# Kernel tuning notes

Measured on AMD Instinct MI355X. Metric: run time of the kernel, lower is better.

The kernel has to match this reference:

```python
import jax, jax.numpy as jnp
import numpy as np

N = 100000      # nodes
E = 3200000     # edges
G = 512         # graphs
F = 12          # num_features
NHID = 64
HGCN = NHID - 3   # 61, GCNConv output dim
EMB_OUT = 64 - F + 2  # 54


def _p(key, shape, scale):
    return jax.random.normal(key, shape, jnp.float32) * scale


def setup_inputs() -> dict:
    key = jax.random.key(0)
    ks = jax.random.split(key, 24)
    inp = {}
    inp["x"] = jax.random.normal(ks[0], (N, F), jnp.float32)
    inp["edge_index"] = jax.random.randint(ks[1], (2, E), 0, N)
    inp["batch"] = jnp.sort(jax.random.randint(ks[2], (N,), 0, G))
    inp["known_mask"] = jax.random.randint(ks[3], (E // 3,), 0, E)
    inp["unk_mask"] = jax.random.randint(ks[4], (E // 3,), 0, E)
    inp["obs_mask"] = jax.random.randint(ks[5], (E // 3,), 0, E)
    inp["fn_averages"] = jax.random.normal(ks[6], (G, 2), jnp.float32)
    inp["infection_rates"] = jax.random.normal(ks[7], (G, 1), jnp.float32)
    # parameters
    inp["msg_weights"] = jax.random.normal(ks[8], (3,), jnp.float32)
    inp["W_emb"] = _p(ks[9], (2, EMB_OUT), 0.5)
    inp["b_emb"] = jnp.zeros((EMB_OUT,), jnp.float32)
    inp["W_gcn"] = _p(ks[10], (64, HGCN), 0.125)
    inp["b_gcn"] = jnp.zeros((HGCN,), jnp.float32)
    inp["W_fn1"] = _p(ks[11], (3, 16), 0.5)
    inp["b_fn1"] = jnp.zeros((16,), jnp.float32)
    inp["W_fn2"] = _p(ks[12], (16, 3), 0.25)
    inp["b_fn2"] = jnp.zeros((3,), jnp.float32)
    inp["W_bb1"] = _p(ks[13], (NHID, NHID), 0.125)
    inp["b_bb1"] = jnp.zeros((NHID,), jnp.float32)
    inp["W_out"] = _p(ks[14], (NHID, 1), 0.125)
    inp["b_out"] = jnp.zeros((1,), jnp.float32)
    return inp


def reference(x, edge_index, batch, known_mask, unk_mask, obs_mask,
              fn_averages, infection_rates, msg_weights,
              W_emb, b_emb, W_gcn, b_gcn, W_fn1, b_fn1, W_fn2, b_fn2,
              W_bb1, b_bb1, W_out, b_out):
    gelu = lambda t: jax.nn.gelu(t, approximate=False)
    n = x.shape[0]
    e = edge_index.shape[1]
    g = fn_averages.shape[0]

    sp = jax.nn.softmax(msg_weights)
    ew = jnp.ones((e,), x.dtype)
    ew = ew.at[known_mask].set(sp[0]).at[unk_mask].set(sp[1]).at[obs_mask].set(sp[2])

    # node embedding: Linear on first 2 feats, concat rest -> (N, 64)
    h = jnp.concatenate([x[:, :2] @ W_emb + b_emb, x[:, 2:]], axis=1)

    # GCNConv(64 -> 61) with edge weights and self-loops
    h = h @ W_gcn                                  # (N, HGCN) transform first
    row, col = edge_index[0], edge_index[1]
    loop = jnp.arange(n)
    row_f = jnp.concatenate([row, loop])
    col_f = jnp.concatenate([col, loop])
    ew_f = jnp.concatenate([ew, jnp.ones((n,), ew.dtype)])
    deg = jax.ops.segment_sum(ew_f, col_f, num_segments=n)   # weighted in-degree
    dis = jnp.where(deg > 0, jax.lax.rsqrt(jnp.maximum(deg, 1e-12)), 0.0)
    norm = dis[row_f] * ew_f * dis[col_f]                    # (E+N,)
    out = jax.ops.segment_sum(norm[:, None] * h[row_f], col_f, num_segments=n)
    out = gelu(out + b_gcn)                                  # dropout = identity (eval)

    # global_add_pool over graphs
    pooled = jax.ops.segment_sum(out, batch, num_segments=g)  # (G, HGCN)

    # fn embeddings MLP on (fn_averages, infection_rate)
    extra = jnp.concatenate([fn_averages.reshape(-1, 2),
                             infection_rates.reshape(-1, 1)], axis=1)  # (G, 3)
    fn_e = gelu(extra @ W_fn1 + b_fn1) @ W_fn2 + b_fn2        # (G, 3)

    z = jnp.concatenate([pooled, fn_e], axis=1)               # (G, NHID)
    z = gelu(z @ W_bb1 + b_bb1)
    logits = z @ W_out + b_out                                # (G, 1)
    return logits
```

## Files before the change

### kernel.cpp

```cpp
#include <hip/hip_runtime.h>
#include <hip/hip_fp16.h>
#include <math.h>

#define F_IN 12
#define NHID 64
#define HGCN 61
#define EMB_OUT 54
#define SCAN_CH 1024
#define PART_R 8192
#define DEG_SCALE 32768.0f
#define NRM_SCALE 32768.0f

typedef unsigned int uint;
typedef unsigned short ushort;
typedef unsigned char uchar;

__device__ __forceinline__ float gelu_exact(float v) {
    return 0.5f * v * (1.0f + erff(v * 0.70710678118654752440f));
}

__device__ __forceinline__ void atomic_add_f32(float* p, float v) {
    unsafeAtomicAdd(p, v);
}

__global__ void prep_kernel(const float* __restrict__ msg_w,
                            const float* __restrict__ W_emb,
                            const float* __restrict__ b_emb,
                            const float* __restrict__ W_gcn,
                            float* __restrict__ sp, uint* __restrict__ spq,
                            float* __restrict__ W_eff, float* __restrict__ b_eff) {
    __shared__ float ssp[4];
    int t = threadIdx.x;
    if (t == 0) {
        float m = fmaxf(msg_w[0], fmaxf(msg_w[1], msg_w[2]));
        float e0 = expf(msg_w[0] - m), e1 = expf(msg_w[1] - m), e2 = expf(msg_w[2] - m);
        float s = e0 + e1 + e2;
        ssp[0] = 1.0f; ssp[1] = e0 / s; ssp[2] = e1 / s; ssp[3] = e2 / s;
        sp[0] = ssp[0]; sp[1] = ssp[1]; sp[2] = ssp[2]; sp[3] = ssp[3];
    }
    __syncthreads();
    if (t < 4) spq[t] = __float2uint_rn(ssp[t] * DEG_SCALE);
    if (t < HGCN) {
        float be = 0.f, w0 = 0.f, w1 = 0.f;
        for (int k = 0; k < EMB_OUT; ++k) {
            float g = W_gcn[k * HGCN + t];
            be += b_emb[k] * g;
            w0 += W_emb[k] * g;
            w1 += W_emb[EMB_OUT + k] * g;
        }
        b_eff[t] = be;
        W_eff[0 * 64 + t] = w0;
        W_eff[1 * 64 + t] = w1;
        for (int f = 2; f < F_IN; ++f)
            W_eff[f * 64 + t] = W_gcn[(EMB_OUT + f - 2) * HGCN + t];
    }
}

__global__ void set_mask_u8(uchar* __restrict__ wclass, const int* __restrict__ mask,
                            uchar v, int n) {
    int i = blockIdx.x * blockDim.x + threadIdx.x;
    if (i < n) wclass[mask[i]] = v;
}

__global__ __launch_bounds__(256) void k1_hist(const int* __restrict__ ei,
                                               uint* __restrict__ H,
                                               uchar* __restrict__ wclass,
                                               int E, int NB, int NBLK) {
    __shared__ uint hist[512];
    int blk = blockIdx.x, t = threadIdx.x;
    hist[t] = 0; hist[t + 256] = 0;
    __syncthreads();
    int lo = blk * PART_R, hi = min(lo + PART_R, E);
    for (int i = lo + t; i < hi; i += 256) {
        wclass[i] = 0;
        atomicAdd(&hist[((uint)ei[E + i]) >> 8], 1u);
    }
    __syncthreads();
    for (int b = t; b < NB; b += 256) H[(size_t)b * NBLK + blk] = hist[b];
}

__global__ void scan_partial_kernel(const int* __restrict__ cnt, int* __restrict__ startv,
                                    int* __restrict__ bsum, int n) {
    __shared__ int s[256];
    int t = threadIdx.x;
    int base = blockIdx.x * SCAN_CH + t * 4;
    int v0 = (base + 0 < n) ? cnt[base + 0] : 0;
    int v1 = (base + 1 < n) ? cnt[base + 1] : 0;
    int v2 = (base + 2 < n) ? cnt[base + 2] : 0;
    int v3 = (base + 3 < n) ? cnt[base + 3] : 0;
    int loc = v0 + v1 + v2 + v3;
    s[t] = loc;
    __syncthreads();
    for (int off = 1; off < 256; off <<= 1) {
        int u = (t >= off) ? s[t - off] : 0;
        __syncthreads();
        s[t] += u;
        __syncthreads();
    }
    int ex = s[t] - loc;
    if (t == 255) bsum[blockIdx.x] = s[255];
    if (base + 0 < n) startv[base + 0] = ex;
    if (base + 1 < n) startv[base + 1] = ex + v0;
    if (base + 2 < n) startv[base + 2] = ex + v0 + v1;
    if (base + 3 < n) startv[base + 3] = ex + v0 + v1 + v2;
}

__global__ void scan_add_kernel(int* __restrict__ startv, const int* __restrict__ bsum, int n) {
    __shared__ int soff;
    int b = blockIdx.x;
    if (threadIdx.x == 0) {
        int q = (b * 256) / SCAN_CH;
        int acc = 0;
        for (int j = 0; j < q; ++j) acc += bsum[j];
        soff = acc;
    }
    __syncthreads();
    int i = b * 256 + threadIdx.x;
    if (i < n) startv[i] += soff;
}

__global__ __launch_bounds__(256) void k3_partition(
        const int* __restrict__ ei, const uchar* __restrict__ wclass,
        const uint* __restrict__ Hs, uint* __restrict__ recSorted,
        int E, int NB, int NBLK) {
    __shared__ uint recs[PART_R];
    __shared__ ushort sbkt[PART_R];
    __shared__ uint hist[512];
    __shared__ uint scanA[512];
    __shared__ uint scanB[512];
    __shared__ int  gbase[512];
    __shared__ uint cursor[512];
    int blk = blockIdx.x, t = threadIdx.x;
    int lo = blk * PART_R, hi = min(lo + PART_R, E);
    int cntTot = hi - lo;
    hist[t] = 0; hist[t + 256] = 0;
    __syncthreads();
    for (int i = lo + t; i < hi; i += 256)
        atomicAdd(&hist[((uint)ei[E + i]) >> 8], 1u);
    __syncthreads();
    uint* src = scanA; uint* dst = scanB;
    src[t] = hist[t]; src[t + 256] = hist[t + 256];
    __syncthreads();
    for (int off = 1; off < 512; off <<= 1) {
        dst[t]       = src[t]       + ((t >= off)       ? src[t - off]       : 0u);
        dst[t + 256] = src[t + 256] + ((t + 256 >= off) ? src[t + 256 - off] : 0u);
        __syncthreads();
        uint* tmp = src; src = dst; dst = tmp;
    }
    uint l0 = (t == 0) ? 0u : src[t - 1];
    uint l1 = src[t + 255];
    cursor[t] = l0; cursor[t + 256] = l1;
    if (t < NB)       gbase[t]       = (int)Hs[(size_t)t * NBLK + blk]         - (int)l0;
    if (t + 256 < NB) gbase[t + 256] = (int)Hs[(size_t)(t + 256) * NBLK + blk] - (int)l1;
    __syncthreads();
    for (int i = lo + t; i < hi; i += 256) {
        uint row = (uint)ei[i];
        uint col = (uint)ei[E + i];
        uint b = col >> 8;
        uint rec = (row << 10) | ((col & 255u) << 2) | (uint)wclass[i];
        uint slot = atomicAdd(&cursor[b], 1u);
        recs[slot] = rec;
        sbkt[slot] = (ushort)b;
    }
    __syncthreads();
    for (int s = t; s < cntTot; s += 256)
        recSorted[gbase[sbkt[s]] + s] = recs[s];
}

__global__ __launch_bounds__(256) void k2_stats(
        const uint* __restrict__ recSorted, const uint* __restrict__ Hs,
        const uint* __restrict__ spq,
        uint* __restrict__ cnt, uint* __restrict__ startv, float* __restrict__ dis,
        int E, int NB, int NBLK, int n_nodes) {
    __shared__ uint hcnt[256], hdeg[256], sA[256], sB[256];
    __shared__ uint sq[4];
    int b = blockIdx.x, t = threadIdx.x;
    hcnt[t] = 0; hdeg[t] = 0;
    if (t < 4) sq[t] = spq[t];
    __syncthreads();
    uint lo = Hs[(size_t)b * NBLK];
    uint hi = (b + 1 < NB) ? Hs[(size_t)(b + 1) * NBLK] : (uint)E;
    for (uint i = lo + t; i < hi; i += 256) {
        uint r = recSorted[i];
        atomicAdd(&hcnt[(r >> 2) & 255u], 1u);
        atomicAdd(&hdeg[(r >> 2) & 255u], sq[r & 3u]);
    }
    __syncthreads();
    uint* src = sA; uint* dst = sB;
    src[t] = hcnt[t];
    __syncthreads();
    for (int off = 1; off < 256; off <<= 1) {
        dst[t] = src[t] + ((t >= off) ? src[t - off] : 0u);
        __syncthreads();
        uint* tmp = src; src = dst; dst = tmp;
    }
    uint excl = (t == 0) ? 0u : src[t - 1];
    int node = (b << 8) + t;
    if (node < n_nodes) {
        cnt[node] = hcnt[t];
        startv[node] = lo + excl;
        float deg = (float)hdeg[t] * (1.0f / DEG_SCALE) + 1.0f;
        dis[node] = rsqrtf(deg);
    }
}

__global__ __launch_bounds__(256) void k4_payload(
        const uint* __restrict__ recSorted, const uint* __restrict__ Hs,
        const float* __restrict__ sp, const float* __restrict__ dis,
        const uint* __restrict__ startv,
        uint* __restrict__ payload, int E, int NB, int NBLK, int n_nodes) {
    __shared__ float disl[256];
    __shared__ uint cur[256];
    __shared__ float spl[4];
    int b = blockIdx.x, t = threadIdx.x;
    int node = (b << 8) + t;
    disl[t] = (node < n_nodes) ? dis[node] : 0.0f;
    cur[t]  = (node < n_nodes) ? startv[node] : 0u;
    if (t < 4) spl[t] = sp[t];
    __syncthreads();
    uint lo = Hs[(size_t)b * NBLK];
    uint hi = (b + 1 < NB) ? Hs[(size_t)(b + 1) * NBLK] : (uint)E;
    for (uint i = lo + t; i < hi; i += 256) {
        uint r = recSorted[i];
        uint row = r >> 10;
        uint c = (r >> 2) & 255u;
        float nrm = dis[row] * spl[r & 3u] * disl[c];
        uint pos = atomicAdd(&cur[c], 1u);
        payload[pos] = (row << 15) | __float2uint_rn(nrm * NRM_SCALE);
    }
}

__global__ void h2_kernel(const float* __restrict__ x, const float* __restrict__ W_eff,
                          const float* __restrict__ b_eff,
                          __half* __restrict__ h2, float* __restrict__ pooled, int g64,
                          int n_nodes) {
    int gid = blockIdx.x * 256 + threadIdx.x;
    if (gid < g64) pooled[gid] = 0.0f;
    int node = blockIdx.x * 4 + (threadIdx.x >> 6);
    int d = threadIdx.x & 63;
    if (node >= n_nodes) return;
    float v = 0.f;
    if (d < HGCN) {
        v = b_eff[d];
#pragma unroll
        for (int f = 0; f < F_IN; ++f)
            v += x[node * F_IN + f] * W_eff[f * 64 + d];
    }
    h2[node * 64 + d] = __float2half(v);
}

__global__ void gather_pool_kernel(const uint* __restrict__ payload,
                                   const uint* __restrict__ startv, const uint* __restrict__ cnt,
                                   const float* __restrict__ dis,
                                   const __half2* __restrict__ h2v,
                                   const float* __restrict__ b_gcn, const int* __restrict__ batch,
                                   float* __restrict__ pooled, int n_nodes) {
    int node = blockIdx.x * 4 + (threadIdx.x >> 6);
    int lane = threadIdx.x & 63;
    int g = lane >> 5;
    int sub = lane & 31;
    if (node >= n_nodes) return;
    int s = (int)startv[node];
    int m = (int)cnt[node];
    const float inv = 1.0f / NRM_SCALE;
    float accx = 0.f, accy = 0.f;
    if (g == 0) {
        float di = dis[node];
        float2 hv = __half22float2(h2v[node * 32 + sub]);
        accx = di * di * hv.x;
        accy = di * di * hv.y;
    }
    for (int j0 = 0; j0 < m; j0 += 64) {
        uint p = 0;
        if (j0 + lane < m) p = payload[s + j0 + lane];
        int lim = min(64, m - j0);
        int npairs = (lim + 1) >> 1;
        int k = 0;
        for (; k + 8 <= npairs; k += 8) {
            uint p0 = __shfl(p, 2 * (k + 0) + g);
            uint p1 = __shfl(p, 2 * (k + 1) + g);
            uint p2 = __shfl(p, 2 * (k + 2) + g);
            uint p3 = __shfl(p, 2 * (k + 3) + g);
            uint p4 = __shfl(p, 2 * (k + 4) + g);
            uint p5 = __shfl(p, 2 * (k + 5) + g);
            uint p6 = __shfl(p, 2 * (k + 6) + g);
            uint p7 = __shfl(p, 2 * (k + 7) + g);
            float2 h0 = __half22float2(h2v[(p0 >> 15) * 32 + sub]);
            float2 h1 = __half22float2(h2v[(p1 >> 15) * 32 + sub]);
            float2 h2f = __half22float2(h2v[(p2 >> 15) * 32 + sub]);
            float2 h3 = __half22float2(h2v[(p3 >> 15) * 32 + sub]);
            float2 h4 = __half22float2(h2v[(p4 >> 15) * 32 + sub]);
            float2 h5 = __half22float2(h2v[(p5 >> 15) * 32 + sub]);
            float2 h6 = __half22float2(h2v[(p6 >> 15) * 32 + sub]);
            float2 h7 = __half22float2(h2v[(p7 >> 15) * 32 + sub]);
            float w0 = (float)(p0 & 32767u) * inv;
            float w1 = (float)(p1 & 32767u) * inv;
            float w2 = (float)(p2 & 32767u) * inv;
            float w3 = (float)(p3 & 32767u) * inv;
            float w4 = (float)(p4 & 32767u) * inv;
            float w5 = (float)(p5 & 32767u) * inv;
            float w6 = (float)(p6 & 32767u) * inv;
            float w7 = (float)(p7 & 32767u) * inv;
            accx += w0 * h0.x; accy += w0 * h0.y;
            accx += w1 * h1.x; accy += w1 * h1.y;
            accx += w2 * h2f.x; accy += w2 * h2f.y;
            accx += w3 * h3.x; accy += w3 * h3.y;
            accx += w4 * h4.x; accy += w4 * h4.y;
            accx += w5 * h5.x; accy += w5 * h5.y;
            accx += w6 * h6.x; accy += w6 * h6.y;
            accx += w7 * h7.x; accy += w7 * h7.y;
        }
        for (; k < npairs; ++k) {
            uint pk = __shfl(p, 2 * k + g);
            float2 hk = __half22float2(h2v[(pk >> 15) * 32 + sub]);
            float wk = (float)(pk & 32767u) * inv;
            accx += wk * hk.x; accy += wk * hk.y;
        }
    }
    accx += __shfl_xor(accx, 32);
    accy += __shfl_xor(accy, 32);
    int d = 2 * sub + g;
    float val = g ? accy : accx;
    if (d < HGCN) {
        float v = gelu_exact(val + b_gcn[d]);
        atomic_add_f32(&pooled[batch[node] * 64 + d], v);
    }
}

__global__ void final_kernel(const float* __restrict__ pooled,
                             const float* __restrict__ fn_avg,
                             const float* __restrict__ inf_rate,
                             const float* __restrict__ W_fn1, const float* __restrict__ b_fn1,
                             const float* __restrict__ W_fn2, const float* __restrict__ b_fn2,
                             const float* __restrict__ W_bb1, const float* __restrict__ b_bb1,
                             const float* __restrict__ W_out, const float* __restrict__ b_out,
                             float* __restrict__ logits) {
    __shared__ float z[64];
    __shared__ float t1[16];
    int g = blockIdx.x;
    int t = threadIdx.x;
    if (t < HGCN) z[t] = pooled[g * 64 + t];
    float e0 = fn_avg[g * 2], e1 = fn_avg[g * 2 + 1], e2 = inf_rate[g];
    if (t < 16) {
        float a = e0 * W_fn1[t] + e1 * W_fn1[16 + t] + e2 * W_fn1[32 + t] + b_fn1[t];
        t1[t] = gelu_exact(a);
    }
    __syncthreads();
    if (t < 3) {
        float a = b_fn2[t];
#pragma unroll
        for (int k = 0; k < 16; ++k) a += t1[k] * W_fn2[k * 3 + t];
        z[HGCN + t] = a;
    }
    __syncthreads();
    float acc = b_bb1[t];
#pragma unroll 8
    for (int k = 0; k < 64; ++k) acc += z[k] * W_bb1[k * 64 + t];
    float p = gelu_exact(acc) * W_out[t];
#pragma unroll
    for (int off = 32; off > 0; off >>= 1) p += __shfl_down(p, off);
    if (t == 0) logits[g] = p + b_out[0];
}

extern "C" void kernel_launch(void* const* d_in, const int* in_sizes, int n_in,
                              void* d_out, int out_size, void* d_ws, size_t ws_size,
                              hipStream_t stream) {
    const float* x        = (const float*)d_in[0];
    const int*   ei       = (const int*)d_in[1];
    const int*   batch    = (const int*)d_in[2];
    const int*   known    = (const int*)d_in[3];
    const int*   unk      = (const int*)d_in[4];
    const int*   obs      = (const int*)d_in[5];
    const float* fn_avg   = (const float*)d_in[6];
    const float* inf_rate = (const float*)d_in[7];
    const float* msg_w    = (const float*)d_in[8];
    const float* W_emb    = (const float*)d_in[9];
    const float* b_emb    = (const float*)d_in[10];
    const float* W_gcn    = (const float*)d_in[11];
    const float* b_gcn    = (const float*)d_in[12];
    const float* W_fn1    = (const float*)d_in[13];
    const float* b_fn1    = (const float*)d_in[14];
    const float* W_fn2    = (const float*)d_in[15];
    const float* b_fn2    = (const float*)d_in[16];
    const float* W_bb1    = (const float*)d_in[17];
    const float* b_bb1    = (const float*)d_in[18];
    const float* W_out    = (const float*)d_in[19];
    const float* b_out    = (const float*)d_in[20];
    float* logits = (float*)d_out;

    const int n_nodes = in_sizes[0] / F_IN;
    const int E       = in_sizes[1] / 2;
    const int nk = in_sizes[3], nu = in_sizes[4], no = in_sizes[5];
    const int G = in_sizes[6] / 2;

    const int NB   = (n_nodes + 255) >> 8;
    const int NBLK = (E + PART_R - 1) / PART_R;
    const int L    = NB * NBLK;
    const int nbL  = (L + SCAN_CH - 1) / SCAN_CH;

    char* ws = (char*)d_ws;
    size_t off = 0;
    auto alloc = [&](size_t bytes) -> void* {
        void* p = ws + off;
        off += (bytes + 255) & ~size_t(255);
        return p;
    };
    uchar*  wclass    = (uchar*)alloc(sizeof(uchar) * (size_t)E);
    uint*   recSorted = (uint*)alloc(sizeof(uint) * (size_t)E);
    uint*   H         = (uint*)alloc(sizeof(uint) * (size_t)L);
    uint*   Hs        = (uint*)alloc(sizeof(uint) * (size_t)L);
    int*    bsum      = (int*)alloc(sizeof(int) * (size_t)(nbL + 1));
    __half* h2        = (__half*)alloc(sizeof(__half) * (size_t)n_nodes * 64);
    uint*   payload   = (uint*)alloc(sizeof(uint) * (size_t)E);
    uint*   cntv      = (uint*)alloc(sizeof(uint) * (size_t)n_nodes);
    uint*   startv    = (uint*)alloc(sizeof(uint) * (size_t)n_nodes);
    float*  dis       = (float*)alloc(sizeof(float) * (size_t)n_nodes);
    float*  pooled    = (float*)alloc(sizeof(float) * (size_t)G * 64);
    float*  W_eff     = (float*)alloc(sizeof(float) * F_IN * 64);
    float*  b_eff     = (float*)alloc(sizeof(float) * 64);
    float*  sp        = (float*)alloc(sizeof(float) * 4);
    uint*   spq       = (uint*)alloc(sizeof(uint) * 4);

    prep_kernel<<<1, 64, 0, stream>>>(msg_w, W_emb, b_emb, W_gcn, sp, spq, W_eff, b_eff);
    k1_hist<<<NBLK, 256, 0, stream>>>(ei, H, wclass, E, NB, NBLK);
    set_mask_u8<<<(nk + 255) / 256, 256, 0, stream>>>(wclass, known, 1, nk);
    set_mask_u8<<<(nu + 255) / 256, 256, 0, stream>>>(wclass, unk, 2, nu);
    set_mask_u8<<<(no + 255) / 256, 256, 0, stream>>>(wclass, obs, 3, no);
    scan_partial_kernel<<<nbL, 256, 0, stream>>>((const int*)H, (int*)Hs, bsum, L);
    scan_add_kernel<<<(L + 255) / 256, 256, 0, stream>>>((int*)Hs, bsum, L);
    k3_partition<<<NBLK, 256, 0, stream>>>(ei, wclass, Hs, recSorted, E, NB, NBLK);
    k2_stats<<<NB, 256, 0, stream>>>(recSorted, Hs, spq, cntv, startv, dis, E, NB, NBLK, n_nodes);
    h2_kernel<<<(n_nodes + 3) / 4, 256, 0, stream>>>(x, W_eff, b_eff, h2, pooled, G * 64, n_nodes);
    k4_payload<<<NB, 256, 0, stream>>>(recSorted, Hs, sp, dis, startv, payload, E, NB, NBLK, n_nodes);
    gather_pool_kernel<<<(n_nodes + 3) / 4, 256, 0, stream>>>(payload, startv, cntv, dis,
                                                              (const __half2*)h2, b_gcn, batch,
                                                              pooled, n_nodes);
    final_kernel<<<G, 64, 0, stream>>>(pooled, fn_avg, inf_rate, W_fn1, b_fn1,
                                       W_fn2, b_fn2, W_bb1, b_bb1, W_out, b_out, logits);
}
```

Measured before the change: 241.9 us.

## Fold degree normalization into node features and merge prep into histogram kernel

Factors the symmetric normalization dis[row]*w*dis[col] so that dis[row] is applied once per source node in h2 and dis[col] once per destination after aggregation. The edge payload then stores only the quantized class weight, which removes the random dis[row] gather per edge in k4_payload. The one-block prep kernel is also merged into block 0 of the histogram kernel, saving a launch. The class weight is quantized at a 16384 scale, and pre-scaling h2 in fp16 changes where rounding happens.

```diff
diff --git a/kernel.cpp b/kernel.cpp
--- a/kernel.cpp
+++ b/kernel.cpp
@@ -9,7 +9,7 @@
 #define SCAN_CH 1024
 #define PART_R 8192
 #define DEG_SCALE 32768.0f
-#define NRM_SCALE 32768.0f
+#define W_SCALE 16384.0f
 
 typedef unsigned int uint;
 typedef unsigned short ushort;
@@ -23,60 +23,57 @@
     unsafeAtomicAdd(p, v);
 }
 
-__global__ void prep_kernel(const float* __restrict__ msg_w,
-                            const float* __restrict__ W_emb,
-                            const float* __restrict__ b_emb,
-                            const float* __restrict__ W_gcn,
-                            float* __restrict__ sp, uint* __restrict__ spq,
-                            float* __restrict__ W_eff, float* __restrict__ b_eff) {
+__global__ __launch_bounds__(256) void k1_hist_prep(
+        const int* __restrict__ ei, uint* __restrict__ H, uchar* __restrict__ wclass,
+        const float* __restrict__ msg_w, const float* __restrict__ W_emb,
+        const float* __restrict__ b_emb, const float* __restrict__ W_gcn,
+        uint* __restrict__ spq, uint* __restrict__ sq15,
+        float* __restrict__ W_eff, float* __restrict__ b_eff,
+        int E, int NB, int NBLK) {
+    __shared__ uint hist[512];
     __shared__ float ssp[4];
-    int t = threadIdx.x;
-    if (t == 0) {
+    int blk = blockIdx.x, t = threadIdx.x;
+    hist[t] = 0; hist[t + 256] = 0;
+    if (blk == 0 && t == 0) {
         float m = fmaxf(msg_w[0], fmaxf(msg_w[1], msg_w[2]));
         float e0 = expf(msg_w[0] - m), e1 = expf(msg_w[1] - m), e2 = expf(msg_w[2] - m);
         float s = e0 + e1 + e2;
         ssp[0] = 1.0f; ssp[1] = e0 / s; ssp[2] = e1 / s; ssp[3] = e2 / s;
-        sp[0] = ssp[0]; sp[1] = ssp[1]; sp[2] = ssp[2]; sp[3] = ssp[3];
-    }
-    __syncthreads();
-    if (t < 4) spq[t] = __float2uint_rn(ssp[t] * DEG_SCALE);
-    if (t < HGCN) {
-        float be = 0.f, w0 = 0.f, w1 = 0.f;
-        for (int k = 0; k < EMB_OUT; ++k) {
-            float g = W_gcn[k * HGCN + t];
-            be += b_emb[k] * g;
-            w0 += W_emb[k] * g;
-            w1 += W_emb[EMB_OUT + k] * g;
+    }
+    __syncthreads();
+    if (blk == 0) {
+        if (t < 4) {
+            spq[t]  = __float2uint_rn(ssp[t] * DEG_SCALE);
+            sq15[t] = __float2uint_rn(ssp[t] * W_SCALE);
         }
-        b_eff[t] = be;
-        W_eff[0 * 64 + t] = w0;
-        W_eff[1 * 64 + t] = w1;
-        for (int f = 2; f < F_IN; ++f)
-            W_eff[f * 64 + t] = W_gcn[(EMB_OUT + f - 2) * HGCN + t];
-    }
+        if (t < HGCN) {
+            float be = 0.f, w0 = 0.f, w1 = 0.f;
+            for (int k = 0; k < EMB_OUT; ++k) {
+                float g = W_gcn[k * HGCN + t];
+                be += b_emb[k] * g;
+                w0 += W_emb[k] * g;
+                w1 += W_emb[EMB_OUT + k] * g;
+            }
+            b_eff[t] = be;
+            W_eff[0 * 64 + t] = w0;
+            W_eff[1 * 64 + t] = w1;
+            for (int f = 2; f < F_IN; ++f)
+                W_eff[f * 64 + t] = W_gcn[(EMB_OUT + f - 2) * HGCN + t];
+        }
+    }
+    int lo = blk * PART_R, hi = min(lo + PART_R, E);
+    for (int i = lo + t; i < hi; i += 256) {
+        wclass[i] = 0;
+        atomicAdd(&hist[((uint)ei[E + i]) >> 8], 1u);
+    }
+    __syncthreads();
+    for (int b = t; b < NB; b += 256) H[(size_t)b * NBLK + blk] = hist[b];
 }
 
 __global__ void set_mask_u8(uchar* __restrict__ wclass, const int* __restrict__ mask,
                             uchar v, int n) {
     int i = blockIdx.x * blockDim.x + threadIdx.x;
     if (i < n) wclass[mask[i]] = v;
-}
-
-__global__ __launch_bounds__(256) void k1_hist(const int* __restrict__ ei,
-                                               uint* __restrict__ H,
-                                               uchar* __restrict__ wclass,
-                                               int E, int NB, int NBLK) {
-    __shared__ uint hist[512];
-    int blk = blockIdx.x, t = threadIdx.x;
-    hist[t] = 0; hist[t + 256] = 0;
-    __syncthreads();
-    int lo = blk * PART_R, hi = min(lo + PART_R, E);
-    for (int i = lo + t; i < hi; i += 256) {
-        wclass[i] = 0;
-        atomicAdd(&hist[((uint)ei[E + i]) >> 8], 1u);
-    }
-    __syncthreads();
-    for (int b = t; b < NB; b += 256) H[(size_t)b * NBLK + blk] = hist[b];
 }
 
 __global__ void scan_partial_kernel(const int* __restrict__ cnt, int* __restrict__ startv,
@@ -206,32 +203,26 @@
 
 __global__ __launch_bounds__(256) void k4_payload(
         const uint* __restrict__ recSorted, const uint* __restrict__ Hs,
-        const float* __restrict__ sp, const float* __restrict__ dis,
-        const uint* __restrict__ startv,
+        const uint* __restrict__ sq15, const uint* __restrict__ startv,
         uint* __restrict__ payload, int E, int NB, int NBLK, int n_nodes) {
-    __shared__ float disl[256];
     __shared__ uint cur[256];
-    __shared__ float spl[4];
+    __shared__ uint wq[4];
     int b = blockIdx.x, t = threadIdx.x;
     int node = (b << 8) + t;
-    disl[t] = (node < n_nodes) ? dis[node] : 0.0f;
-    cur[t]  = (node < n_nodes) ? startv[node] : 0u;
-    if (t < 4) spl[t] = sp[t];
+    cur[t] = (node < n_nodes) ? startv[node] : 0u;
+    if (t < 4) wq[t] = sq15[t];
     __syncthreads();
     uint lo = Hs[(size_t)b * NBLK];
     uint hi = (b + 1 < NB) ? Hs[(size_t)(b + 1) * NBLK] : (uint)E;
     for (uint i = lo + t; i < hi; i += 256) {
         uint r = recSorted[i];
-        uint row = r >> 10;
-        uint c = (r >> 2) & 255u;
-        float nrm = dis[row] * spl[r & 3u] * disl[c];
-        uint pos = atomicAdd(&cur[c], 1u);
-        payload[pos] = (row << 15) | __float2uint_rn(nrm * NRM_SCALE);
+        uint pos = atomicAdd(&cur[(r >> 2) & 255u], 1u);
+        payload[pos] = ((r >> 10) << 15) | wq[r & 3u];
     }
 }
 
 __global__ void h2_kernel(const float* __restrict__ x, const float* __restrict__ W_eff,
-                          const float* __restrict__ b_eff,
+                          const float* __restrict__ b_eff, const float* __restrict__ dis,
                           __half* __restrict__ h2, float* __restrict__ pooled, int g64,
                           int n_nodes) {
     int gid = blockIdx.x * 256 + threadIdx.x;
@@ -245,6 +236,7 @@
 #pragma unroll
         for (int f = 0; f < F_IN; ++f)
             v += x[node * F_IN + f] * W_eff[f * 64 + d];
+        v *= dis[node];
     }
     h2[node * 64 + d] = __float2half(v);
 }
@@ -262,13 +254,12 @@
     if (node >= n_nodes) return;
     int s = (int)startv[node];
     int m = (int)cnt[node];
-    const float inv = 1.0f / NRM_SCALE;
+    const float inv = 1.0f / W_SCALE;
     float accx = 0.f, accy = 0.f;
     if (g == 0) {
-        float di = dis[node];
         float2 hv = __half22float2(h2v[node * 32 + sub]);
-        accx = di * di * hv.x;
-        accy = di * di * hv.y;
+        accx = hv.x;
+        accy = hv.y;
     }
     for (int j0 = 0; j0 < m; j0 += 64) {
         uint p = 0;
@@ -320,7 +311,7 @@
     accx += __shfl_xor(accx, 32);
     accy += __shfl_xor(accy, 32);
     int d = 2 * sub + g;
-    float val = g ? accy : accx;
+    float val = (g ? accy : accx) * dis[node];
     if (d < HGCN) {
         float v = gelu_exact(val + b_gcn[d]);
         atomic_add_f32(&pooled[batch[node] * 64 + d], v);
@@ -418,11 +409,11 @@
     float*  pooled    = (float*)alloc(sizeof(float) * (size_t)G * 64);
     float*  W_eff     = (float*)alloc(sizeof(float) * F_IN * 64);
     float*  b_eff     = (float*)alloc(sizeof(float) * 64);
-    float*  sp        = (float*)alloc(sizeof(float) * 4);
     uint*   spq       = (uint*)alloc(sizeof(uint) * 4);
-
-    prep_kernel<<<1, 64, 0, stream>>>(msg_w, W_emb, b_emb, W_gcn, sp, spq, W_eff, b_eff);
-    k1_hist<<<NBLK, 256, 0, stream>>>(ei, H, wclass, E, NB, NBLK);
+    uint*   sq15      = (uint*)alloc(sizeof(uint) * 4);
+
+    k1_hist_prep<<<NBLK, 256, 0, stream>>>(ei, H, wclass, msg_w, W_emb, b_emb, W_gcn,
+                                           spq, sq15, W_eff, b_eff, E, NB, NBLK);
     set_mask_u8<<<(nk + 255) / 256, 256, 0, stream>>>(wclass, known, 1, nk);
     set_mask_u8<<<(nu + 255) / 256, 256, 0, stream>>>(wclass, unk, 2, nu);
     set_mask_u8<<<(no + 255) / 256, 256, 0, stream>>>(wclass, obs, 3, no);
@@ -430,8 +421,9 @@
     scan_add_kernel<<<(L + 255) / 256, 256, 0, stream>>>((int*)Hs, bsum, L);
     k3_partition<<<NBLK, 256, 0, stream>>>(ei, wclass, Hs, recSorted, E, NB, NBLK);
     k2_stats<<<NB, 256, 0, stream>>>(recSorted, Hs, spq, cntv, startv, dis, E, NB, NBLK, n_nodes);
-    h2_kernel<<<(n_nodes + 3) / 4, 256, 0, stream>>>(x, W_eff, b_eff, h2, pooled, G * 64, n_nodes);
-    k4_payload<<<NB, 256, 0, stream>>>(recSorted, Hs, sp, dis, startv, payload, E, NB, NBLK, n_nodes);
+    h2_kernel<<<(n_nodes + 3) / 4, 256, 0, stream>>>(x, W_eff, b_eff, dis, h2, pooled,
+                                                     G * 64, n_nodes);
+    k4_payload<<<NB, 256, 0, stream>>>(recSorted, Hs, sq15, startv, payload, E, NB, NBLK, n_nodes);
     gather_pool_kernel<<<(n_nodes + 3) / 4, 256, 0, stream>>>(payload, startv, cntv, dis,
                                                               (const __half2*)h2, b_gcn, batch,
                                                               pooled, n_nodes);
```

Result: faster. 228.8 us (-5.4%).
